# Kernel tuning notes

Hardware: AMD Instinct MI355X
Metric: run time of the kernel (lower is better)

The kernel has to match this reference:

```python
import jax, jax.numpy as jnp
import numpy as np

N = 8192
IN_DIM = 512
MEM_DIM = 512


def _linear_params(k, fan_in, fan_out):
    kw, kb = jax.random.split(k)
    s = 1.0 / np.sqrt(fan_in)
    W = jax.random.uniform(kw, (fan_in, fan_out), jnp.float32, -s, s)
    b = jax.random.uniform(kb, (fan_out,), jnp.float32, -s, s)
    return W, b


def setup_inputs() -> dict:
    key = jax.random.key(0)
    ks = jax.random.split(key, 12)
    inputs = jax.random.normal(ks[0], (N, IN_DIM), jnp.float32)
    # tree.type is a [1,2] mixing matrix per node (lang vs vis weights)
    type_mask = jax.nn.softmax(jax.random.normal(ks[1], (N, 2), jnp.float32), axis=-1)
    # topologically ordered tree: parent slot of node i is in [0, i]; slot 0 = virtual zero root state
    rng = np.random.default_rng(0)
    parent = np.zeros(N, dtype=np.int32)
    for i in range(1, N):
        parent[i] = rng.integers(0, i + 1)
    d = {"inputs": inputs, "type_mask": type_mask, "parent": jnp.asarray(parent)}
    names = ["ioux_vis", "iouh_vis", "fx_vis", "fh_vis",
             "ioux_lang", "iouh_lang", "fx_lang", "fh_lang"]
    fanins = [IN_DIM, MEM_DIM, IN_DIM, MEM_DIM] * 2
    fanouts = [3 * MEM_DIM, 3 * MEM_DIM, MEM_DIM, MEM_DIM] * 2
    for j, nm in enumerate(names):
        W, b = _linear_params(ks[2 + j], fanins[j], fanouts[j])
        d["W_" + nm] = W
        d["b_" + nm] = b
    return d


def reference(inputs, type_mask, parent,
              W_ioux_vis, b_ioux_vis, W_iouh_vis, b_iouh_vis,
              W_fx_vis, b_fx_vis, W_fh_vis, b_fh_vis,
              W_ioux_lang, b_ioux_lang, W_iouh_lang, b_iouh_lang,
              W_fx_lang, b_fx_lang, W_fh_lang, b_fh_lang):
    n_nodes = inputs.shape[0]
    D = W_fh_vis.shape[1]
    # batch the input-dependent projections into big GEMMs (fused across all nodes)
    x_iou_v = inputs @ W_ioux_vis + b_ioux_vis  # [N, 3D]
    x_f_v = inputs @ W_fx_vis + b_fx_vis        # [N, D]
    x_iou_l = inputs @ W_ioux_lang + b_ioux_lang
    x_f_l = inputs @ W_fx_lang + b_fx_lang

    def node(x_iou, x_f, h_p, c_p, W_iouh, b_iouh, W_fh, b_fh):
        iou = x_iou + h_p @ W_iouh + b_iouh  # [3D]
        i, o, u = jnp.split(iou, 3)
        f = jax.nn.sigmoid(x_f + h_p @ W_fh + b_fh)
        c = jax.nn.sigmoid(i) * jnp.tanh(u) + f * c_p
        h = jax.nn.sigmoid(o) * jnp.tanh(c)
        return c, h

    # slot 0 holds the zero state used by root nodes; node i lives at slot i+1
    c0 = jnp.zeros((n_nodes + 1, D), inputs.dtype)
    h0 = jnp.zeros((n_nodes + 1, D), inputs.dtype)

    def step(carry, xs):
        c_all, h_all = carry
        n, p, xiv, xfv, xil, xfl, tm = xs
        h_p = h_all[p]
        c_p = c_all[p]
        c_v, h_v = node(xiv, xfv, h_p, c_p, W_iouh_vis, b_iouh_vis, W_fh_vis, b_fh_vis)
        c_l, h_l = node(xil, xfl, h_p, c_p, W_iouh_lang, b_iouh_lang, W_fh_lang, b_fh_lang)
        # type_mask @ cat([lang, vis]) == tm[0]*lang + tm[1]*vis
        c_n = tm[0] * c_l + tm[1] * c_v
        h_n = tm[0] * h_l + tm[1] * h_v  # dropout is identity in eval
        return (c_all.at[n + 1].set(c_n), h_all.at[n + 1].set(h_n)), None

    idx = jnp.arange(n_nodes)
    (c_all, h_all), _ = jax.lax.scan(
        step, (c0, h0), (idx, parent, x_iou_v, x_f_v, x_iou_l, x_f_l, type_mask))
    return c_all[1:], h_all[1:]
```

## Files before the change

### kernel.cpp

```cpp
#include <hip/hip_runtime.h>
#include <math.h>

typedef unsigned short ushort_t;
typedef unsigned int uint_t;
typedef unsigned long long u64_t;
typedef __attribute__((ext_vector_type(8))) short short8;
typedef __attribute__((ext_vector_type(4))) float f32x4;

#define N_NODES 8192
#define DIM 512
#define KTOT 1024
#define NCOLS 4096
#define BM 128
#define BN 128
#define NTILE (NCOLS / BN)
#define KIT (KTOT / 32)
#define WIMG_USHORTS ((size_t)NTILE * KIT * 4096)
#define MAXLEV_LDS 128

__device__ __forceinline__ float sigm(float x) { return 1.0f / (1.0f + __expf(-x)); }
__device__ __forceinline__ float tanh_fast(float x) {
    float ax = fabsf(x);
    float e = __expf(2.0f * ax);
    float t = 1.0f - 2.0f / (e + 1.0f);
    return copysignf(t, x);
}
__device__ __forceinline__ uint_t packf(float f) {
    uint_t u = __float_as_uint(f);
    uint_t hi = u & 0xffff0000u;
    float r = f - __uint_as_float(hi);
    return hi | (__float_as_uint(r) >> 16);
}
__device__ __forceinline__ uint_t rne16(float f) {
    uint_t u = __float_as_uint(f);
    return (u + 0x7fffu + ((u >> 16) & 1u)) >> 16;
}

__device__ __forceinline__ void fragAB_u32(const uint4 w0, const uint4 w1,
                                           short8& hi8, short8& lo8) {
    union { uint_t w[4]; short8 s; } H, L;
    uint_t u[8] = { w0.x, w0.y, w0.z, w0.w, w1.x, w1.y, w1.z, w1.w };
#pragma unroll
    for (int j = 0; j < 4; ++j) {
        H.w[j] = (u[2 * j + 1] & 0xffff0000u) | (u[2 * j] >> 16);
        L.w[j] = (u[2 * j + 1] << 16) | (u[2 * j] & 0xffffu);
    }
    hi8 = H.s; lo8 = L.s;
}

__device__ __forceinline__ void fragA_f32(const float4 f0, const float4 f1,
                                          short8& hi8, short8& lo8) {
    union { uint_t w[4]; short8 s; } H, L;
    float f[8] = { f0.x, f0.y, f0.z, f0.w, f1.x, f1.y, f1.z, f1.w };
#pragma unroll
    for (int j = 0; j < 4; ++j) {
        float a = f[2 * j], b = f[2 * j + 1];
        uint_t h0 = __float_as_uint(a) & 0xffff0000u;
        uint_t h1 = __float_as_uint(b) & 0xffff0000u;
        float r0 = a - __uint_as_float(h0);
        float r1 = b - __uint_as_float(h1);
        H.w[j] = h1 | (h0 >> 16);
        L.w[j] = (__float_as_uint(r1) & 0xffff0000u) | (__float_as_uint(r0) >> 16);
    }
    hi8 = H.s; lo8 = L.s;
}

__global__ void __launch_bounds__(256) prep_wimg_kernel(
    const float* __restrict__ Wx_iou_v, const float* __restrict__ Wh_iou_v,
    const float* __restrict__ Wx_f_v,   const float* __restrict__ Wh_f_v,
    const float* __restrict__ Wx_iou_l, const float* __restrict__ Wh_iou_l,
    const float* __restrict__ Wx_f_l,   const float* __restrict__ Wh_f_l,
    ushort_t* __restrict__ Wimg)
{
    __shared__ float T[32][132];
    int p = blockIdx.x >> 5, it = blockIdx.x & 31;
    int tid = threadIdx.x;
#pragma unroll
    for (int e = 0; e < 16; ++e) {
        int lin = e * 256 + tid;
        int dloc = lin & 15, kk = (lin >> 4) & 31, q = lin >> 9;
        int d = p * 16 + dloc;
        int qq = q & 3; bool lang = q >= 4;
        int k = it * 32 + kk;
        const float* W; int col, stride;
        if (qq < 3) { col = qq * DIM + d; stride = 3 * DIM;
            W = (k < DIM) ? (lang ? Wx_iou_l : Wx_iou_v) : (lang ? Wh_iou_l : Wh_iou_v); }
        else        { col = d; stride = DIM;
            W = (k < DIM) ? (lang ? Wx_f_l : Wx_f_v) : (lang ? Wh_f_l : Wh_f_v); }
        int kr = (k < DIM) ? k : (k - DIM);
        T[kk][dloc * 8 + q] = W[(size_t)kr * stride + col];
    }
    __syncthreads();
    size_t tilebase = (size_t)blockIdx.x * 4096;
#pragma unroll
    for (int gch = 0; gch < 2; ++gch) {
        int gi = gch * 256 + tid;
        int col = gi >> 2, gd = gi & 3;
        uint_t wds[4];
#pragma unroll
        for (int i = 0; i < 4; ++i) {
            uint_t v0 = rne16(T[gd * 8 + 2 * i][col]);
            uint_t v1 = rne16(T[gd * 8 + 2 * i + 1][col]);
            wds[i] = (v1 << 16) | v0;
        }
        *(uint4*)(Wimg + tilebase + (size_t)gi * 8) = make_uint4(wds[0], wds[1], wds[2], wds[3]);
    }
}

__global__ void prep_bias_kernel(
    const float* __restrict__ bx_iou_v, const float* __restrict__ bh_iou_v,
    const float* __restrict__ bx_f_v,   const float* __restrict__ bh_f_v,
    const float* __restrict__ bx_iou_l, const float* __restrict__ bh_iou_l,
    const float* __restrict__ bx_f_l,   const float* __restrict__ bh_f_l,
    float* __restrict__ bias)
{
    int j = blockIdx.x * blockDim.x + threadIdx.x;
    if (j >= NCOLS) return;
    int d = j >> 3, q = j & 7;
    int qq = q & 3;
    bool lang = (q & 4) != 0;
    const float* bx; const float* bh; int col;
    if (qq < 3) { col = qq * DIM + d; bx = lang ? bx_iou_l : bx_iou_v; bh = lang ? bh_iou_l : bh_iou_v; }
    else        { col = d;            bx = lang ? bx_f_l  : bx_f_v;   bh = lang ? bh_f_l  : bh_f_v; }
    bias[j] = bx[col] + bh[col];
}

__global__ void __launch_bounds__(1024) levels_sort_kernel(
    const int* __restrict__ parent,
    int* __restrict__ order, int* __restrict__ offsets,
    int* __restrict__ counts, int* __restrict__ cursors,
    int* __restrict__ nlev, int* __restrict__ tilestart,
    int* __restrict__ rbStart, int* __restrict__ nodeHrb)
{
    __shared__ int s_level[N_NODES];
    __shared__ int s_assigned;
    __shared__ int s_maxlev;
    int tid = threadIdx.x;
    int pr[8];
#pragma unroll
    for (int ii = 0; ii < 8; ++ii) {
        int i = tid + ii * 1024;
        pr[ii] = parent[i];
        s_level[i] = -1;
    }
    for (int i = tid; i <= N_NODES; i += 1024) counts[i] = 0;
    if (tid == 0) { s_assigned = 0; s_maxlev = 0; }
    __syncthreads();

    for (int pass = 0; pass <= N_NODES; ++pass) {
        int newly = 0;
#pragma unroll
        for (int ii = 0; ii < 8; ++ii) {
            int i = tid + ii * 1024;
            if (s_level[i] < 0) {
                int p = pr[ii];
                if (p == 0) { s_level[i] = 0; newly++; }
                else { int lp = s_level[p - 1]; if (lp >= 0) { s_level[i] = lp + 1; newly++; } }
            }
        }
        if (newly) atomicAdd(&s_assigned, newly);
        __syncthreads();
        int a = s_assigned;
        if (a >= N_NODES) break;
        __syncthreads();
    }

#pragma unroll
    for (int ii = 0; ii < 8; ++ii) {
        int i = tid + ii * 1024;
        int lv = s_level[i];
        atomicAdd(&counts[lv], 1);
        atomicMax(&s_maxlev, lv);
    }
    __syncthreads();
    if (tid == 0) {
        int nl = s_maxlev + 1;
        nlev[0] = nl;
        int off = 0, toff = 0, rb = 0;
        for (int l = 0; l < nl; ++l) {
            offsets[l] = off; cursors[l] = off;
            tilestart[l] = toff; rbStart[l] = rb;
            int mt = (counts[l] + BM - 1) / BM;
            rb += mt;
            toff += mt * NTILE;
            off += counts[l];
        }
        offsets[nl] = off;
        tilestart[nl] = toff;
        rbStart[nl] = rb;
        nlev[1] = toff;
    }
    __syncthreads();
#pragma unroll
    for (int ii = 0; ii < 8; ++ii) {
        int i = tid + ii * 1024;
        int lv = s_level[i];
        int pos = atomicAdd(&cursors[lv], 1);
        order[pos] = i;
        nodeHrb[i] = rbStart[lv] + ((pos - offsets[lv]) >> 7);
    }
}

__global__ void __launch_bounds__(256, 2) tree_fused_kernel(
    const float* __restrict__ inputs, const float* __restrict__ type_mask,
    const ushort_t* __restrict__ Wimg, const float* __restrict__ bias,
    const int* __restrict__ order, const int* __restrict__ offsets,
    const int* __restrict__ nlev, const int* __restrict__ parent,
    const int* __restrict__ rbStart,
    int* __restrict__ colCnt,
    uint_t* __restrict__ hPack, uint_t* __restrict__ cPack,
    float* __restrict__ out)
{
    float* cOut = out;
    float* hOut = out + (size_t)N_NODES * DIM;

    __shared__ float eps[BM * 68];
    __shared__ int s_node[BM];
    __shared__ int s_par[BM];
    __shared__ float s_tm[BM][2];
    __shared__ int s_rbs[MAXLEV_LDS];
    __shared__ int s_off[MAXLEV_LDS];
    __shared__ int s_cok[32];
    __shared__ int s_ok[8];

    int tid = threadIdx.x;
    int lane = tid & 63, w = tid >> 6, wr = w >> 1, wc = w & 1;
    int l15 = lane & 15, g = lane >> 4;
    int nl = nlev[0];
    int total = nlev[1];

    int nload = nl + 1; if (nload > MAXLEV_LDS) nload = MAXLEV_LDS;
    for (int i = tid; i < nload; i += 256) { s_rbs[i] = rbStart[i]; s_off[i] = offsets[i]; }
    __syncthreads();

    const ushort_t* bLane = Wimg + (size_t)(wc * 64 + l15) * 32 + (size_t)g * 8;

#define LDB(RB, tilebase, itt) { \
    _Pragma("unroll") for (int n_ = 0; n_ < 4; ++n_) \
        RB[n_] = *(const uint4*)(bLane + (size_t)(tilebase + (itt)) * 4096 + n_ * 512); }

#define LDA_H(RA, itrel) { \
    _Pragma("unroll") for (int m_ = 0; m_ < 4; ++m_) { \
        const uint4* p_ = (const uint4*)(aBaseH[m_] + (itrel) * 32 + g * 8); \
        RA[m_][0] = p_[0]; RA[m_][1] = p_[1]; } }

#define LDA_X(RA, itt) { \
    _Pragma("unroll") for (int m_ = 0; m_ < 4; ++m_) { \
        const float4* p_ = (const float4*)(aBaseX[m_] + (itt) * 32 + g * 8); \
        RA[m_][0] = p_[0]; RA[m_][1] = p_[1]; } }

#define COMP_H(RA, RB) { \
    short8 bh_[4]; \
    _Pragma("unroll") for (int n_ = 0; n_ < 4; ++n_) { \
        union { uint4 u; short8 s; } c_; c_.u = RB[n_]; bh_[n_] = c_.s; } \
    _Pragma("unroll") for (int m_ = 0; m_ < 4; ++m_) { \
        short8 ah_, al_; fragAB_u32(RA[m_][0], RA[m_][1], ah_, al_); \
        _Pragma("unroll") for (int n_ = 0; n_ < 4; ++n_) { \
            acc[m_][n_] = __builtin_amdgcn_mfma_f32_16x16x32_bf16(ah_, bh_[n_], acc[m_][n_], 0, 0, 0); \
            acc[m_][n_] = __builtin_amdgcn_mfma_f32_16x16x32_bf16(al_, bh_[n_], acc[m_][n_], 0, 0, 0); } } }

#define COMP_X(RA, RB) { \
    short8 bh_[4]; \
    _Pragma("unroll") for (int n_ = 0; n_ < 4; ++n_) { \
        union { uint4 u; short8 s; } c_; c_.u = RB[n_]; bh_[n_] = c_.s; } \
    _Pragma("unroll") for (int m_ = 0; m_ < 4; ++m_) { \
        short8 ah_, al_; fragA_f32(RA[m_][0], RA[m_][1], ah_, al_); \
        _Pragma("unroll") for (int n_ = 0; n_ < 4; ++n_) { \
            acc[m_][n_] = __builtin_amdgcn_mfma_f32_16x16x32_bf16(ah_, bh_[n_], acc[m_][n_], 0, 0, 0); \
            acc[m_][n_] = __builtin_amdgcn_mfma_f32_16x16x32_bf16(al_, bh_[n_], acc[m_][n_], 0, 0, 0); } } }

#define WAIT_GROUPS(colPrev, nPrev, gq) { \
    for (;;) { \
        if (tid < 32) \
            s_cok[tid] = (__hip_atomic_load(&(colPrev)[tid], __ATOMIC_RELAXED, \
                                            __HIP_MEMORY_SCOPE_AGENT) >= (nPrev)) ? 1 : 0; \
        __syncthreads(); \
        if (tid < 8) { \
            if (s_cok[4 * tid] && s_cok[4 * tid + 1] && s_cok[4 * tid + 2] && s_cok[4 * tid + 3]) \
                s_ok[tid] = 1; \
        } \
        __syncthreads(); \
        if (s_ok[gq]) break; \
        __builtin_amdgcn_s_sleep(8); \
    } }

    for (int t = blockIdx.x; t < total; t += gridDim.x) {
        int lev = 0;
        while (lev + 1 < nload && s_rbs[lev + 1] * NTILE <= t) ++lev;
        int lt = t - s_rbs[lev] * NTILE;
        int ntile = lt % NTILE;
        int mt = lt / NTILE;
        int start = s_off[lev];
        int cnt = s_off[lev + 1] - start;
        int jc = ntile * BN;
        int r0 = mt * BM;
        int tbx = ntile * KIT;
        int tbh = ntile * KIT + 16;

        if (tid < BM) {
            int r = r0 + tid;
            int node = (r < cnt) ? order[start + r] : -1;
            s_node[tid] = node;
            int p = (node >= 0) ? parent[node] : 0;
            s_par[tid] = p;
            float t0 = 0.f, t1 = 0.f;
            if (node >= 0) { t0 = type_mask[node * 2]; t1 = type_mask[node * 2 + 1]; }
            s_tm[tid][0] = t0; s_tm[tid][1] = t1;
        }
        if (tid < 32) s_cok[tid] = 0;
        if (tid < 8) s_ok[tid] = 0;
        __syncthreads();

        f32x4 acc[4][4];
#pragma unroll
        for (int m = 0; m < 4; ++m)
#pragma unroll
            for (int n = 0; n < 4; ++n) acc[m][n] = (f32x4)(0.f);

        {
            const float* aBaseX[4];
#pragma unroll
            for (int m = 0; m < 4; ++m) {
                int nd = s_node[wr * 64 + m * 16 + l15];
                aBaseX[m] = inputs + (size_t)(nd < 0 ? 0 : nd) * DIM;
            }
            float4 xa0[4][2], xa1[4][2]; uint4 xb0[4], xb1[4];
            LDA_X(xa0, 0); LDB(xb0, tbx, 0);
#pragma unroll
            for (int ii = 0; ii < 8; ++ii) {
                int e = 2 * ii, o = e + 1;
                LDA_X(xa1, o); LDB(xb1, tbx, o);
                __builtin_amdgcn_s_setprio(1);
                COMP_X(xa0, xb0);
                __builtin_amdgcn_s_setprio(0);
                if (e + 2 < 16) { LDA_X(xa0, e + 2); LDB(xb0, tbx, e + 2); }
                __builtin_amdgcn_s_setprio(1);
                COMP_X(xa1, xb1);
                __builtin_amdgcn_s_setprio(0);
            }
        }

        if (lev > 0) {
            const int* colPrev = colCnt + (lev - 1) * NTILE;
            int nPrev = s_rbs[lev] - s_rbs[lev - 1];

            uint4 ha0[4][2], ha1[4][2]; uint4 hb0[4], hb1[4];
            LDB(hb0, tbh, 0); LDB(hb1, tbh, 1);

            WAIT_GROUPS(colPrev, nPrev, 0);

            const uint_t* aBaseH[4];
#pragma unroll
            for (int m = 0; m < 4; ++m) {
                int p = s_par[wr * 64 + m * 16 + l15];
                aBaseH[m] = hPack + (size_t)((p > 0) ? (p - 1) : 0) * DIM;
            }
            LDA_H(ha0, 0); LDA_H(ha1, 1);
#pragma unroll
            for (int ii = 0; ii < 8; ++ii) {
                int e = 2 * ii, o = e + 1;
                __builtin_amdgcn_s_setprio(1);
                COMP_H(ha0, hb0);
                __builtin_amdgcn_s_setprio(0);
                if (ii < 7) {
                    if (!s_ok[ii + 1]) WAIT_GROUPS(colPrev, nPrev, ii + 1);
                    LDA_H(ha0, e + 2); LDB(hb0, tbh, e + 2);
                }
                __builtin_amdgcn_s_setprio(1);
                COMP_H(ha1, hb1);
                __builtin_amdgcn_s_setprio(0);
                if (ii < 7) { LDA_H(ha1, o + 2); LDB(hb1, tbh, o + 2); }
            }
        }

        int cntloc = cnt - r0; if (cntloc > BM) cntloc = BM;
        __syncthreads();
#pragma unroll
        for (int pass = 0; pass < 2; ++pass) {
            if (wc == pass) {
#pragma unroll
                for (int m = 0; m < 4; ++m)
#pragma unroll
                    for (int n = 0; n < 4; ++n) {
                        int row = wr * 64 + m * 16 + g * 4;
                        int c = n * 16 + l15;
#pragma unroll
                        for (int r = 0; r < 4; ++r) eps[(row + r) * 68 + c] = acc[m][n][r];
                    }
            }
            __syncthreads();
#pragma unroll
            for (int e = 0; e < 4; ++e) {
                int task = e * 256 + tid;
                int row = task >> 3, dl = task & 7;
                if (row < cntloc) {
                    int node = s_node[row]; int p = s_par[row];
                    const float* ep = &eps[row * 68 + dl * 8];
                    float4 v0 = *(const float4*)ep;
                    float4 v1 = *(const float4*)(ep + 4);
                    int jb = jc + pass * 64 + dl * 8;
                    float4 b0 = *(const float4*)(bias + jb);
                    float4 b1 = *(const float4*)(bias + jb + 4);
                    int d = jb >> 3;
                    float cp = 0.f;
                    if (p > 0) {
                        uint_t wrd = cPack[(size_t)(p - 1) * DIM + d];
                        cp = __uint_as_float(wrd & 0xffff0000u) + __uint_as_float(wrd << 16);
                    }
                    float cv = sigm(v0.x + b0.x) * tanh_fast(v0.z + b0.z)
                             + sigm(v0.w + b0.w) * cp;
                    float hv = sigm(v0.y + b0.y) * tanh_fast(cv);
                    float cl = sigm(v1.x + b1.x) * tanh_fast(v1.z + b1.z)
                             + sigm(v1.w + b1.w) * cp;
                    float hl = sigm(v1.y + b1.y) * tanh_fast(cl);
                    float tm0 = s_tm[row][0], tm1 = s_tm[row][1];
                    float cn = tm0 * cl + tm1 * cv;
                    float hn2 = tm0 * hl + tm1 * hv;
                    size_t oi = (size_t)node * DIM + d;
                    __hip_atomic_store(&cPack[oi], packf(cn),
                                       __ATOMIC_RELAXED, __HIP_MEMORY_SCOPE_AGENT);
                    __hip_atomic_store(&hPack[oi], packf(hn2),
                                       __ATOMIC_RELAXED, __HIP_MEMORY_SCOPE_AGENT);
                    cOut[oi] = cn;
                    hOut[oi] = hn2;
                }
            }
            __syncthreads();
        }

        __builtin_amdgcn_s_waitcnt(0);
        __syncthreads();
        if (tid == 0)
            __hip_atomic_fetch_add(&colCnt[lev * NTILE + ntile], 1,
                                   __ATOMIC_RELAXED, __HIP_MEMORY_SCOPE_AGENT);
    }
#undef LDB
#undef LDA_H
#undef LDA_X
#undef COMP_H
#undef COMP_X
#undef WAIT_GROUPS
}

extern "C" void kernel_launch(void* const* d_in, const int* in_sizes, int n_in,
                              void* d_out, int out_size, void* d_ws, size_t ws_size,
                              hipStream_t stream) {
    const float* inputs      = (const float*)d_in[0];
    const float* type_mask   = (const float*)d_in[1];
    const int*   parent      = (const int*)d_in[2];
    const float* W_ioux_vis  = (const float*)d_in[3];
    const float* b_ioux_vis  = (const float*)d_in[4];
    const float* W_iouh_vis  = (const float*)d_in[5];
    const float* b_iouh_vis  = (const float*)d_in[6];
    const float* W_fx_vis    = (const float*)d_in[7];
    const float* b_fx_vis    = (const float*)d_in[8];
    const float* W_fh_vis    = (const float*)d_in[9];
    const float* b_fh_vis    = (const float*)d_in[10];
    const float* W_ioux_lang = (const float*)d_in[11];
    const float* b_ioux_lang = (const float*)d_in[12];
    const float* W_iouh_lang = (const float*)d_in[13];
    const float* b_iouh_lang = (const float*)d_in[14];
    const float* W_fx_lang   = (const float*)d_in[15];
    const float* b_fx_lang   = (const float*)d_in[16];
    const float* W_fh_lang   = (const float*)d_in[17];
    const float* b_fh_lang   = (const float*)d_in[18];

    ushort_t* Wimg = (ushort_t*)d_ws;
    float* bias    = (float*)(Wimg + WIMG_USHORTS);
    int* order     = (int*)(bias + NCOLS);
    int* offsets   = order + N_NODES;
    int* counts    = offsets + (N_NODES + 2);
    int* cursors   = counts + (N_NODES + 2);
    int* nlev      = cursors + (N_NODES + 2);
    int* tilestart = nlev + 8;
    int* rbStart   = tilestart + (N_NODES + 2);
    int* nodeHrb   = rbStart + (N_NODES + 2);
    int* colCnt    = nodeHrb + N_NODES;
    size_t off2 = (size_t)((char*)(colCnt + MAXLEV_LDS * NTILE) - (char*)d_ws);
    off2 = (off2 + 255) & ~(size_t)255;
    uint_t* hPack = (uint_t*)((char*)d_ws + off2);
    uint_t* cPack = hPack + (size_t)N_NODES * DIM;

    float* out = (float*)d_out;

    hipMemsetAsync((void*)colCnt, 0, MAXLEV_LDS * NTILE * sizeof(int), stream);

    hipLaunchKernelGGL(prep_wimg_kernel, dim3(NTILE * KIT), dim3(256), 0, stream,
                       W_ioux_vis, W_iouh_vis, W_fx_vis, W_fh_vis,
                       W_ioux_lang, W_iouh_lang, W_fx_lang, W_fh_lang, Wimg);
    hipLaunchKernelGGL(prep_bias_kernel, dim3(NCOLS / 256), dim3(256), 0, stream,
                       b_ioux_vis, b_iouh_vis, b_fx_vis, b_fh_vis,
                       b_ioux_lang, b_iouh_lang, b_fx_lang, b_fh_lang, bias);
    hipLaunchKernelGGL(levels_sort_kernel, dim3(1), dim3(1024), 0, stream,
                       parent, order, offsets, counts, cursors, nlev, tilestart,
                       rbStart, nodeHrb);

    int occ = 0;
    if (hipOccupancyMaxActiveBlocksPerMultiprocessor(&occ, (const void*)tree_fused_kernel, 256, 0) != hipSuccess || occ < 1)
        occ = 1;
    int bpc = occ < 2 ? occ : 2;
    dim3 grid(256 * bpc);

    void* args[] = { (void*)&inputs, (void*)&type_mask, (void*)&Wimg, (void*)&bias,
                     (void*)&order, (void*)&offsets, (void*)&nlev, (void*)&parent,
                     (void*)&rbStart, (void*)&colCnt,
                     (void*)&hPack, (void*)&cPack, (void*)&out };
    hipLaunchCooperativeKernel((const void*)tree_fused_kernel, grid, dim3(256), args, 0, stream);
}
```

Before: 815.1 us.

## Rotate recurrent K-group order, single-pass epilogue, defer fp32 output stores past signal

Each tile now starts the recurrent h-GEMM at the K-group matching its own column group (ntile>>2) and rotates through the rest. The aim is to consume first the parent columns most likely finished, instead of always waiting on group 0. The epilogue stages the whole 128x128 accumulator in one LDS pass (larger eps buffer) and prefetches the parent c values before the barrier. The fp32 cOut/hOut writes move after the colCnt increment, so dependent tiles are released sooner. The spin sleep is also shortened. The larger LDS buffer may reduce occupancy.

```diff
diff --git a/kernel.cpp b/kernel.cpp
--- a/kernel.cpp
+++ b/kernel.cpp
@@ -30,6 +30,9 @@
     uint_t hi = u & 0xffff0000u;
     float r = f - __uint_as_float(hi);
     return hi | (__float_as_uint(r) >> 16);
+}
+__device__ __forceinline__ float unpackw(uint_t w) {
+    return __uint_as_float(w & 0xffff0000u) + __uint_as_float(w << 16);
 }
 __device__ __forceinline__ uint_t rne16(float f) {
     uint_t u = __float_as_uint(f);
@@ -214,7 +217,7 @@
     float* cOut = out;
     float* hOut = out + (size_t)N_NODES * DIM;
 
-    __shared__ float eps[BM * 68];
+    __shared__ float eps[BM * 132];
     __shared__ int s_node[BM];
     __shared__ int s_par[BM];
     __shared__ float s_tm[BM][2];
@@ -281,7 +284,7 @@
         } \
         __syncthreads(); \
         if (s_ok[gq]) break; \
-        __builtin_amdgcn_s_sleep(8); \
+        __builtin_amdgcn_s_sleep(4); \
     } }
 
     for (int t = blockIdx.x; t < total; t += gridDim.x) {
@@ -343,11 +346,7 @@
         if (lev > 0) {
             const int* colPrev = colCnt + (lev - 1) * NTILE;
             int nPrev = s_rbs[lev] - s_rbs[lev - 1];
-
-            uint4 ha0[4][2], ha1[4][2]; uint4 hb0[4], hb1[4];
-            LDB(hb0, tbh, 0); LDB(hb1, tbh, 1);
-
-            WAIT_GROUPS(colPrev, nPrev, 0);
+            const int gb = ntile >> 2;
 
             const uint_t* aBaseH[4];
 #pragma unroll
@@ -355,77 +354,87 @@
                 int p = s_par[wr * 64 + m * 16 + l15];
                 aBaseH[m] = hPack + (size_t)((p > 0) ? (p - 1) : 0) * DIM;
             }
-            LDA_H(ha0, 0); LDA_H(ha1, 1);
-#pragma unroll
-            for (int ii = 0; ii < 8; ++ii) {
-                int e = 2 * ii, o = e + 1;
+
+            uint4 ha0[4][2], ha1[4][2]; uint4 hb0[4], hb1[4];
+            WAIT_GROUPS(colPrev, nPrev, gb);
+            LDA_H(ha0, 2 * gb); LDB(hb0, tbh, 2 * gb);
+            LDA_H(ha1, 2 * gb + 1); LDB(hb1, tbh, 2 * gb + 1);
+#pragma unroll
+            for (int s = 0; s < 8; ++s) {
+                const int gn = (gb + s + 1) & 7;
                 __builtin_amdgcn_s_setprio(1);
                 COMP_H(ha0, hb0);
                 __builtin_amdgcn_s_setprio(0);
-                if (ii < 7) {
-                    if (!s_ok[ii + 1]) WAIT_GROUPS(colPrev, nPrev, ii + 1);
-                    LDA_H(ha0, e + 2); LDB(hb0, tbh, e + 2);
+                if (s < 7) {
+                    if (!s_ok[gn]) WAIT_GROUPS(colPrev, nPrev, gn);
+                    LDA_H(ha0, 2 * gn); LDB(hb0, tbh, 2 * gn);
                 }
                 __builtin_amdgcn_s_setprio(1);
                 COMP_H(ha1, hb1);
                 __builtin_amdgcn_s_setprio(0);
-                if (ii < 7) { LDA_H(ha1, o + 2); LDB(hb1, tbh, o + 2); }
+                if (s < 7) { LDA_H(ha1, 2 * gn + 1); LDB(hb1, tbh, 2 * gn + 1); }
             }
         }
 
         int cntloc = cnt - r0; if (cntloc > BM) cntloc = BM;
+
+        float CP[8];
+#pragma unroll
+        for (int e = 0; e < 8; ++e) {
+            int task = e * 256 + tid;
+            int row = task >> 4, dl = task & 15;
+            CP[e] = 0.f;
+            if (row < cntloc) {
+                int p = s_par[row];
+                if (p > 0) {
+                    int d = (jc + dl * 8) >> 3;
+                    CP[e] = unpackw(cPack[(size_t)(p - 1) * DIM + d]);
+                }
+            }
+        }
+
+#pragma unroll
+        for (int m = 0; m < 4; ++m)
+#pragma unroll
+            for (int n = 0; n < 4; ++n) {
+                int row = wr * 64 + m * 16 + g * 4;
+                int c = wc * 64 + n * 16 + l15;
+#pragma unroll
+                for (int r = 0; r < 4; ++r) eps[(row + r) * 132 + c] = acc[m][n][r];
+            }
         __syncthreads();
-#pragma unroll
-        for (int pass = 0; pass < 2; ++pass) {
-            if (wc == pass) {
-#pragma unroll
-                for (int m = 0; m < 4; ++m)
-#pragma unroll
-                    for (int n = 0; n < 4; ++n) {
-                        int row = wr * 64 + m * 16 + g * 4;
-                        int c = n * 16 + l15;
-#pragma unroll
-                        for (int r = 0; r < 4; ++r) eps[(row + r) * 68 + c] = acc[m][n][r];
-                    }
-            }
-            __syncthreads();
-#pragma unroll
-            for (int e = 0; e < 4; ++e) {
-                int task = e * 256 + tid;
-                int row = task >> 3, dl = task & 7;
-                if (row < cntloc) {
-                    int node = s_node[row]; int p = s_par[row];
-                    const float* ep = &eps[row * 68 + dl * 8];
-                    float4 v0 = *(const float4*)ep;
-                    float4 v1 = *(const float4*)(ep + 4);
-                    int jb = jc + pass * 64 + dl * 8;
-                    float4 b0 = *(const float4*)(bias + jb);
-                    float4 b1 = *(const float4*)(bias + jb + 4);
-                    int d = jb >> 3;
-                    float cp = 0.f;
-                    if (p > 0) {
-                        uint_t wrd = cPack[(size_t)(p - 1) * DIM + d];
-                        cp = __uint_as_float(wrd & 0xffff0000u) + __uint_as_float(wrd << 16);
-                    }
-                    float cv = sigm(v0.x + b0.x) * tanh_fast(v0.z + b0.z)
-                             + sigm(v0.w + b0.w) * cp;
-                    float hv = sigm(v0.y + b0.y) * tanh_fast(cv);
-                    float cl = sigm(v1.x + b1.x) * tanh_fast(v1.z + b1.z)
-                             + sigm(v1.w + b1.w) * cp;
-                    float hl = sigm(v1.y + b1.y) * tanh_fast(cl);
-                    float tm0 = s_tm[row][0], tm1 = s_tm[row][1];
-                    float cn = tm0 * cl + tm1 * cv;
-                    float hn2 = tm0 * hl + tm1 * hv;
-                    size_t oi = (size_t)node * DIM + d;
-                    __hip_atomic_store(&cPack[oi], packf(cn),
-                                       __ATOMIC_RELAXED, __HIP_MEMORY_SCOPE_AGENT);
-                    __hip_atomic_store(&hPack[oi], packf(hn2),
-                                       __ATOMIC_RELAXED, __HIP_MEMORY_SCOPE_AGENT);
-                    cOut[oi] = cn;
-                    hOut[oi] = hn2;
-                }
-            }
-            __syncthreads();
+
+        float CN[8], HN[8];
+#pragma unroll
+        for (int e = 0; e < 8; ++e) {
+            int task = e * 256 + tid;
+            int row = task >> 4, dl = task & 15;
+            CN[e] = 0.f; HN[e] = 0.f;
+            if (row < cntloc) {
+                int node = s_node[row];
+                const float* ep = &eps[row * 132 + dl * 8];
+                float4 v0 = *(const float4*)ep;
+                float4 v1 = *(const float4*)(ep + 4);
+                int jb = jc + dl * 8;
+                float4 b0 = *(const float4*)(bias + jb);
+                float4 b1 = *(const float4*)(bias + jb + 4);
+                float cp = CP[e];
+                float cv = sigm(v0.x + b0.x) * tanh_fast(v0.z + b0.z)
+                         + sigm(v0.w + b0.w) * cp;
+                float hv = sigm(v0.y + b0.y) * tanh_fast(cv);
+                float cl = sigm(v1.x + b1.x) * tanh_fast(v1.z + b1.z)
+                         + sigm(v1.w + b1.w) * cp;
+                float hl = sigm(v1.y + b1.y) * tanh_fast(cl);
+                float tm0 = s_tm[row][0], tm1 = s_tm[row][1];
+                float cn = tm0 * cl + tm1 * cv;
+                float hn2 = tm0 * hl + tm1 * hv;
+                CN[e] = cn; HN[e] = hn2;
+                size_t oi = (size_t)node * DIM + (jb >> 3);
+                __hip_atomic_store(&cPack[oi], packf(cn),
+                                   __ATOMIC_RELAXED, __HIP_MEMORY_SCOPE_AGENT);
+                __hip_atomic_store(&hPack[oi], packf(hn2),
+                                   __ATOMIC_RELAXED, __HIP_MEMORY_SCOPE_AGENT);
+            }
         }
 
         __builtin_amdgcn_s_waitcnt(0);
@@ -433,6 +442,19 @@
         if (tid == 0)
             __hip_atomic_fetch_add(&colCnt[lev * NTILE + ntile], 1,
                                    __ATOMIC_RELAXED, __HIP_MEMORY_SCOPE_AGENT);
+
+#pragma unroll
+        for (int e = 0; e < 8; ++e) {
+            int task = e * 256 + tid;
+            int row = task >> 4, dl = task & 15;
+            if (row < cntloc) {
+                int node = s_node[row];
+                size_t oi = (size_t)node * DIM + ((jc + dl * 8) >> 3);
+                cOut[oi] = CN[e];
+                hOut[oi] = HN[e];
+            }
+        }
+        __syncthreads();
     }
 #undef LDB
 #undef LDA_H
```

Result: no change. 807.8 us (-0.9%).
